# Performance work log

Hardware: AMD Instinct MI355X
Metric: run time of the kernel (lower is better)

Reference implementation:

```python
import jax, jax.numpy as jnp
import numpy as np

N_BUS = 4096
BATCH = 1024


def setup_inputs() -> dict:
    key = jax.random.key(0)
    ks = jax.random.split(key, 10)
    u = jax.random.normal(ks[0], (BATCH, N_BUS), dtype=jnp.float32)
    w = jax.random.normal(ks[1], (BATCH, N_BUS), dtype=jnp.float32)
    # parameters (torch.rand -> uniform[0,1); Linear init ~ U(-1/sqrt(n), 1/sqrt(n)))
    G = jax.random.uniform(ks[2], (N_BUS, N_BUS), dtype=jnp.float32)
    B = jax.random.uniform(ks[3], (N_BUS, N_BUS), dtype=jnp.float32)
    bias_p = jax.random.uniform(ks[4], (1, N_BUS), dtype=jnp.float32)
    bias_q = jax.random.uniform(ks[5], (1, N_BUS), dtype=jnp.float32)
    lim = 1.0 / np.sqrt(N_BUS)
    Wp = jax.random.uniform(ks[6], (N_BUS, N_BUS), dtype=jnp.float32, minval=-lim, maxval=lim)
    bp = jax.random.uniform(ks[7], (N_BUS,), dtype=jnp.float32, minval=-lim, maxval=lim)
    Wq = jax.random.uniform(ks[8], (N_BUS, N_BUS), dtype=jnp.float32, minval=-lim, maxval=lim)
    bq = jax.random.uniform(ks[9], (N_BUS,), dtype=jnp.float32, minval=-lim, maxval=lim)
    return {"u": u, "w": w, "G": G, "B": B, "bias_p": bias_p, "bias_q": bias_q,
            "Wp": Wp, "bp": bp, "Wq": Wq, "bq": bq}


def reference(u, w, G, B, bias_p, bias_q, Wp, bp, Wq, bq):
    # Algebraically identical to the original's outer-product form:
    # p_i = sum_k (u_i u_k + w_i w_k) G_ik + (w_i u_k - u_i w_k) B_ik
    #     = u_i (G u)_i + w_i (G w)_i + w_i (B u)_i - u_i (B w)_i
    # q_i = sum_k (w_i u_k - u_i w_k) G_ik - (u_i u_k + w_i w_k) B_ik
    #     = w_i (G u)_i - u_i (G w)_i - u_i (B u)_i - w_i (B w)_i
    Gu = u @ G.T  # (batch, n_bus): (G u)_i = sum_k G_ik u_k
    Gw = w @ G.T
    Bu = u @ B.T
    Bw = w @ B.T
    p = u * Gu + w * Gw + w * Bu - u * Bw + bias_p
    q = w * Gu - u * Gw - u * Bu - w * Bw + bias_q
    # nn.Linear: y = x @ W^T + b
    p = p @ Wp.T + bp
    q = q @ Wq.T + bq
    return (p, q)
```

## Files before the change

kernel.cpp:

```cpp
#include <hip/hip_runtime.h>
#include <hip/hip_bf16.h>

#define NB 4096
#define MB 1024
#define SZ ((size_t)MB * NB)
#define NN ((size_t)NB * NB)

typedef __bf16 bf16_t;
typedef __attribute__((ext_vector_type(8))) __bf16 bf16x8;
typedef __attribute__((ext_vector_type(4))) float f32x4;
typedef __attribute__((ext_vector_type(4))) unsigned int u32x4;

#define AS1 __attribute__((address_space(1)))
#define AS3 __attribute__((address_space(3)))
#define GLOAD16(gp, lp)                                                        \
  __builtin_amdgcn_global_load_lds((const AS1 unsigned int*)(gp),              \
                                   (AS3 unsigned int*)(lp), 16, 0, 0)
#define SBAR() __builtin_amdgcn_s_barrier()
#define SCHEDB() __builtin_amdgcn_sched_barrier(0)
#define MFMA16(a, b, c) __builtin_amdgcn_mfma_f32_16x16x32_bf16((a), (b), (c), 0, 0, 0)
#define VMCNT4() asm volatile("s_waitcnt vmcnt(4)" ::: "memory")
#define VMCNT0() asm volatile("s_waitcnt vmcnt(0)" ::: "memory")


__device__ __forceinline__ bf16x8 neg8(bf16x8 x) {
  u32x4 t;
  __builtin_memcpy(&t, &x, 16);
  t ^= 0x80008000u;
  bf16x8 y;
  __builtin_memcpy(&y, &t, 16);
  return y;
}

__device__ __forceinline__ bf16x8 cvt8(float4 a, float4 b) {
  bf16x8 v;
  v[0] = (bf16_t)a.x; v[1] = (bf16_t)a.y; v[2] = (bf16_t)a.z; v[3] = (bf16_t)a.w;
  v[4] = (bf16_t)b.x; v[5] = (bf16_t)b.y; v[6] = (bf16_t)b.z; v[7] = (bf16_t)b.w;
  return v;
}

#define ITEM_S (SZ / 8)
#define ITEM_N (NN / 8)

__global__ __launch_bounds__(256) void prep6_kernel(
    const float* __restrict__ u, const float* __restrict__ w,
    const float* __restrict__ G, const float* __restrict__ Bm,
    const float* __restrict__ Wp, const float* __restrict__ Wq,
    bf16_t* __restrict__ ws) {
  size_t stride = (size_t)gridDim.x * blockDim.x;
  const size_t tot = 2 * ITEM_S + 4 * ITEM_N;
  for (size_t i = (size_t)blockIdx.x * blockDim.x + threadIdx.x; i < tot;
       i += stride) {
    const float* src;
    bf16_t* dst;
    size_t off;
    if (i < ITEM_S) { src = u; dst = ws; off = i; }
    else if (i < 2 * ITEM_S) { src = w; dst = ws + SZ; off = i - ITEM_S; }
    else if (i < 2 * ITEM_S + ITEM_N) { src = G; dst = ws + 2 * SZ; off = i - 2 * ITEM_S; }
    else if (i < 2 * ITEM_S + 2 * ITEM_N) { src = Bm; dst = ws + 2 * SZ + NN; off = i - 2 * ITEM_S - ITEM_N; }
    else if (i < 2 * ITEM_S + 3 * ITEM_N) { src = Wp; dst = ws + 2 * SZ + 2 * NN; off = i - 2 * ITEM_S - 2 * ITEM_N; }
    else { src = Wq; dst = ws + 2 * SZ + 3 * NN; off = i - 2 * ITEM_S - 3 * ITEM_N; }
    const float4* s = reinterpret_cast<const float4*>(src) + off * 2;
    reinterpret_cast<bf16x8*>(dst)[off] = cvt8(s[0], s[1]);
  }
}

__global__ __launch_bounds__(256) void prep4_kernel(
    const float* __restrict__ u, const float* __restrict__ w,
    const float* __restrict__ G, const float* __restrict__ Bm,
    bf16_t* __restrict__ ws) {
  size_t stride = (size_t)gridDim.x * blockDim.x;
  const size_t tot = 2 * ITEM_S + 2 * ITEM_N;
  for (size_t i = (size_t)blockIdx.x * blockDim.x + threadIdx.x; i < tot;
       i += stride) {
    const float* src;
    bf16_t* dst;
    size_t off;
    if (i < ITEM_S) { src = u; dst = ws; off = i; }
    else if (i < 2 * ITEM_S) { src = w; dst = ws + SZ; off = i - ITEM_S; }
    else if (i < 2 * ITEM_S + ITEM_N) { src = G; dst = ws + 2 * SZ; off = i - 2 * ITEM_S; }
    else { src = Bm; dst = ws + 2 * SZ + NN; off = i - 2 * ITEM_S - ITEM_N; }
    const float4* s = reinterpret_cast<const float4*>(src) + off * 2;
    reinterpret_cast<bf16x8*>(dst)[off] = cvt8(s[0], s[1]);
  }
}

__global__ __launch_bounds__(256, 2) void fused1_v9(
    const float* __restrict__ u, const float* __restrict__ w,
    const bf16_t* __restrict__ ubf, const bf16_t* __restrict__ wbf,
    const bf16_t* __restrict__ Gbf, const bf16_t* __restrict__ Bbf,
    const float* __restrict__ bias_p, const float* __restrict__ bias_q,
    bf16_t* __restrict__ pq) {
  __shared__ bf16_t lds[2][4][128 * 32];
  const int tid = threadIdx.x, lane = tid & 63, wv = tid >> 6;
  const int bid = blockIdx.x;
  const int t = (bid & 7) * 32 + (bid >> 3);
  const int row0 = (t & 7) * 128, col0 = (t >> 3) * 128;
  const int koff = (bid & 1) << 6;
  const int wm = (wv >> 1) * 64, wn = (wv & 1) * 64;
  const int lr = lane & 15, kq = lane >> 4;
  const int kswz = (kq ^ ((lr >> 1) & 3)) << 3;

  const int srow = tid >> 2;
  const int sc = (tid & 3) ^ ((tid >> 3) & 3);
  const bf16_t* gsA[4];
  const bf16_t* gsB[4];
  {
    const bf16_t* bases[4] = {ubf, wbf, Gbf, Bbf};
    const int r0s[4] = {row0, row0, col0, col0};
#pragma unroll
    for (int o = 0; o < 4; ++o) {
      gsA[o] = bases[o] + (size_t)(r0s[o] + srow) * NB + sc * 8;
      gsB[o] = gsA[o] + (size_t)64 * NB;
    }
  }

#define F1_ISSUE(hh)                                                          \
  do {                                                                        \
    const int _sl = (hh) & 1;                                                 \
    const int _ko = (((hh) + koff) & 127) * 32;                               \
    _Pragma("unroll") for (int _o = 0; _o < 4; ++_o) {                        \
      GLOAD16(gsA[_o] + _ko, &lds[_sl][_o][wv * 512]);                        \
      GLOAD16(gsB[_o] + _ko, &lds[_sl][_o][2048 + wv * 512]);                 \
    }                                                                         \
  } while (0)

  int aoff[4], boff[4];
#pragma unroll
  for (int m = 0; m < 4; ++m) aoff[m] = (wm + m * 16 + lr) * 32 + kswz;
#pragma unroll
  for (int n = 0; n < 4; ++n) boff[n] = (wn + n * 16 + lr) * 32 + kswz;

  f32x4 aS[4][4] = {}, aT[4][4] = {};

  F1_ISSUE(0);
  VMCNT0();
  __syncthreads();

  for (int h = 0; h < 128; ++h) {
    const int slot = h & 1;
    bf16x8 au[4], aw[4], bG[4], bB[4];
#pragma unroll
    for (int m = 0; m < 4; ++m) {
      au[m] = *reinterpret_cast<const bf16x8*>(&lds[slot][0][aoff[m]]);
      aw[m] = *reinterpret_cast<const bf16x8*>(&lds[slot][1][aoff[m]]);
    }
#pragma unroll
    for (int n = 0; n < 4; ++n) {
      bG[n] = *reinterpret_cast<const bf16x8*>(&lds[slot][2][boff[n]]);
      bB[n] = *reinterpret_cast<const bf16x8*>(&lds[slot][3][boff[n]]);
    }
    if (h + 1 < 128) F1_ISSUE(h + 1);
#pragma unroll
    for (int n = 0; n < 4; ++n) {
      bf16x8 bn = neg8(bB[n]);
#pragma unroll
      for (int m = 0; m < 4; ++m) {
        aS[m][n] = MFMA16(au[m], bG[n], aS[m][n]);
        aS[m][n] = MFMA16(aw[m], bn, aS[m][n]);
        aT[m][n] = MFMA16(aw[m], bG[n], aT[m][n]);
        aT[m][n] = MFMA16(au[m], bB[n], aT[m][n]);
      }
    }
    if (h + 1 < 128) {
      VMCNT0();
      SBAR();
      SCHEDB();
    }
  }

  const int fr = lane & 15, fq = kq;
#pragma unroll
  for (int m = 0; m < 4; ++m)
#pragma unroll
    for (int n = 0; n < 4; ++n)
#pragma unroll
      for (int j = 0; j < 4; ++j) {
        int r = row0 + wm + m * 16 + fq * 4 + j;
        int c = col0 + wn + n * 16 + fr;
        size_t idx = (size_t)r * NB + c;
        float U = u[idx], W = w[idx];
        float S = aS[m][n][j], T = aT[m][n][j];
        pq[idx] = (bf16_t)(U * S + W * T + bias_p[c]);
        pq[SZ + idx] = (bf16_t)(W * S - U * T + bias_q[c]);
      }
}

__global__ __launch_bounds__(256, 2) void gemm2_v9(
    const bf16_t* __restrict__ pq, const bf16_t* __restrict__ Wpb,
    const bf16_t* __restrict__ Wqb, const float* __restrict__ bp,
    const float* __restrict__ bq, float* __restrict__ out) {
  __shared__ bf16_t lds[4][2][128 * 32];
  const int tid = threadIdx.x, lane = tid & 63, wv = tid >> 6;
  const int bid = blockIdx.x;
  const int t = (bid & 7) * 64 + (bid >> 3);
  const int z = t >> 8;
  const int s = t & 255;
  const int row0 = (s & 7) * 128, col0 = (s >> 3) * 128;
  const int koff = (bid & 1) << 6;

  const bf16_t* A = pq + (size_t)z * SZ;
  const bf16_t* Wm = z ? Wqb : Wpb;
  const float* bias = z ? bq : bp;
  float* C = out + (size_t)z * SZ;

  const int wm = (wv >> 1) * 64, wn = (wv & 1) * 64;
  const int lr = lane & 15, kq = lane >> 4;
  const int kswz = (kq ^ ((lr >> 1) & 3)) << 3;

  const int srow = tid >> 2;
  const int sc = (tid & 3) ^ ((tid >> 3) & 3);
  const bf16_t* gA0 = A + (size_t)(row0 + srow) * NB + sc * 8;
  const bf16_t* gA1 = gA0 + (size_t)64 * NB;
  const bf16_t* gW0 = Wm + (size_t)(col0 + srow) * NB + sc * 8;
  const bf16_t* gW1 = gW0 + (size_t)64 * NB;

#define G2_ISSUE(hh)                                                           \
  do {                                                                         \
    const int _sl = (hh) & 3;                                                  \
    const int _ko = (((hh) + koff) & 127) * 32;                                \
    GLOAD16(gA0 + _ko, &lds[_sl][0][wv * 512]);                                \
    GLOAD16(gA1 + _ko, &lds[_sl][0][2048 + wv * 512]);                         \
    GLOAD16(gW0 + _ko, &lds[_sl][1][wv * 512]);                                \
    GLOAD16(gW1 + _ko, &lds[_sl][1][2048 + wv * 512]);                         \
  } while (0)

  int aoff[4], woff[4];
#pragma unroll
  for (int m = 0; m < 4; ++m) aoff[m] = (wm + m * 16 + lr) * 32 + kswz;
#pragma unroll
  for (int n = 0; n < 4; ++n) woff[n] = (wn + n * 16 + lr) * 32 + kswz;

  f32x4 acc[4][4] = {};

  G2_ISSUE(0); G2_ISSUE(1); G2_ISSUE(2);
  VMCNT4();
  SBAR();
  SCHEDB();

  const int HTOT = 2 * (NB / 64);
  for (int h = 0; h < HTOT; ++h) {
    const int slot = h & 3;
    const bool pf = (h + 3) < HTOT;

    bf16x8 av[4], bw[4];
#pragma unroll
    for (int m = 0; m < 4; ++m)
      av[m] = *reinterpret_cast<const bf16x8*>(&lds[slot][0][aoff[m]]);
#pragma unroll
    for (int n = 0; n < 4; ++n)
      bw[n] = *reinterpret_cast<const bf16x8*>(&lds[slot][1][woff[n]]);
    if (pf) G2_ISSUE(h + 3);
#pragma unroll
    for (int m = 0; m < 4; ++m)
#pragma unroll
      for (int n = 0; n < 4; ++n)
        acc[m][n] = MFMA16(av[m], bw[n], acc[m][n]);
    if (h < HTOT - 3)
      VMCNT4();
    else if (h == HTOT - 3)
      asm volatile("s_waitcnt vmcnt(2)" ::: "memory");
    else if (h == HTOT - 2)
      VMCNT0();
    SBAR();
    SCHEDB();
  }

  const int fr = lane & 15, fq = kq;
#pragma unroll
  for (int m = 0; m < 4; ++m)
#pragma unroll
    for (int n = 0; n < 4; ++n)
#pragma unroll
      for (int j = 0; j < 4; ++j) {
        int r = row0 + wm + m * 16 + fq * 4 + j;
        int c = col0 + wn + n * 16 + fr;
        C[(size_t)r * NB + c] = acc[m][n][j] + bias[c];
      }
}

__device__ __forceinline__ int swz_off32(int r, int kk) {
  return r * 32 + ((kk ^ ((r >> 1) & 3)) << 3);
}

__device__ __forceinline__ void fb_stage_f32(const float* __restrict__ src,
                                             int row0, int k0, bf16_t* lds, int t) {
  int r = t >> 2, kk = t & 3;
  const float* p = src + (size_t)(row0 + r) * NB + k0 + (kk << 3);
  float4 v0 = *reinterpret_cast<const float4*>(p);
  float4 v1 = *reinterpret_cast<const float4*>(p + 4);
  *reinterpret_cast<bf16x8*>(lds + swz_off32(r, kk)) = cvt8(v0, v1);
}

__global__ __launch_bounds__(256, 2) void fb_gemm2(
    const bf16_t* __restrict__ pq, const float* __restrict__ Wp,
    const float* __restrict__ Wq, const float* __restrict__ bp,
    const float* __restrict__ bq, float* __restrict__ out) {
  __shared__ bf16_t lA[128 * 32], lW[128 * 32];
  const int z = blockIdx.z;
  const bf16_t* A = pq + (size_t)z * SZ;
  const float* Wm = z ? Wq : Wp;
  const float* bias = z ? bq : bp;
  float* C = out + (size_t)z * SZ;
  const int tid = threadIdx.x;
  const int lane = tid & 63, wv = tid >> 6;
  const int wm = (wv >> 1) * 64, wn = (wv & 1) * 64;
  const int row0 = blockIdx.y * 128, col0 = blockIdx.x * 128;
  const int lr = lane & 15, kq = lane >> 4;
  const int fslot = (kq ^ ((lr >> 1) & 3)) << 3;
  f32x4 acc[4][4] = {};
  for (int kt = 0; kt < NB; kt += 32) {
#pragma unroll
    for (int p = 0; p < 2; ++p) {
      int cb = p * 256 + wv * 64;
      int ci = cb + lane;
      int r = ci >> 2, kl = ci & 3;
      int ks = kl ^ ((r >> 1) & 3);
      const bf16_t* g = A + (size_t)(row0 + r) * NB + kt + (ks << 3);
      GLOAD16(g, lA + cb * 8);
    }
#pragma unroll
    for (int p = 0; p < 2; ++p)
      fb_stage_f32(Wm, col0, kt, lW, p * 256 + tid);
    __syncthreads();
    bf16x8 af[4], bg[4];
#pragma unroll
    for (int m = 0; m < 4; ++m)
      af[m] = *reinterpret_cast<const bf16x8*>(lA + (wm + m * 16 + lr) * 32 + fslot);
#pragma unroll
    for (int n = 0; n < 4; ++n)
      bg[n] = *reinterpret_cast<const bf16x8*>(lW + (wn + n * 16 + lr) * 32 + fslot);
#pragma unroll
    for (int m = 0; m < 4; ++m)
#pragma unroll
      for (int n = 0; n < 4; ++n)
        acc[m][n] = MFMA16(af[m], bg[n], acc[m][n]);
    __syncthreads();
  }
  const int fr = lane & 15, fq = lane >> 4;
#pragma unroll
  for (int m = 0; m < 4; ++m)
#pragma unroll
    for (int n = 0; n < 4; ++n)
#pragma unroll
      for (int j = 0; j < 4; ++j) {
        int r = row0 + wm + m * 16 + fq * 4 + j;
        int c = col0 + wn + n * 16 + fr;
        C[(size_t)r * NB + c] = acc[m][n][j] + bias[c];
      }
}

__global__ __launch_bounds__(512, 2) void fb_fused1(
    const float* __restrict__ u, const float* __restrict__ w,
    const float* __restrict__ G, const float* __restrict__ Bm,
    const float* __restrict__ bias_p, const float* __restrict__ bias_q,
    bf16_t* __restrict__ pq) {
  __shared__ bf16_t lU[128 * 32], lW[128 * 32], lG[128 * 32], lB[128 * 32];
  const int tid = threadIdx.x;
  const int lane = tid & 63, wv = tid >> 6;
  const int wm = (wv >> 2) * 64, wn = (wv & 3) * 32;
  const int row0 = blockIdx.y * 128, col0 = blockIdx.x * 128;
  const int lr = lane & 15, kq = lane >> 4;
  const int fslot = (kq ^ ((lr >> 1) & 3)) << 3;
  f32x4 aS[4][2] = {}, aT[4][2] = {};
  for (int kt = 0; kt < NB; kt += 32) {
    fb_stage_f32(u, row0, kt, lU, tid);
    fb_stage_f32(w, row0, kt, lW, tid);
    fb_stage_f32(G, col0, kt, lG, tid);
    fb_stage_f32(Bm, col0, kt, lB, tid);
    __syncthreads();
    bf16x8 au[4], aw[4], bG[2], bB[2], bBn[2];
#pragma unroll
    for (int m = 0; m < 4; ++m) {
      int off = (wm + m * 16 + lr) * 32 + fslot;
      au[m] = *reinterpret_cast<const bf16x8*>(lU + off);
      aw[m] = *reinterpret_cast<const bf16x8*>(lW + off);
    }
#pragma unroll
    for (int n = 0; n < 2; ++n) {
      int off = (wn + n * 16 + lr) * 32 + fslot;
      bG[n] = *reinterpret_cast<const bf16x8*>(lG + off);
      bB[n] = *reinterpret_cast<const bf16x8*>(lB + off);
      bBn[n] = neg8(bB[n]);
    }
#pragma unroll
    for (int m = 0; m < 4; ++m)
#pragma unroll
      for (int n = 0; n < 2; ++n) {
        aS[m][n] = MFMA16(au[m], bG[n], aS[m][n]);
        aS[m][n] = MFMA16(aw[m], bBn[n], aS[m][n]);
        aT[m][n] = MFMA16(aw[m], bG[n], aT[m][n]);
        aT[m][n] = MFMA16(au[m], bB[n], aT[m][n]);
      }
    __syncthreads();
  }
  const int fr = lane & 15, fq = lane >> 4;
#pragma unroll
  for (int m = 0; m < 4; ++m)
#pragma unroll
    for (int n = 0; n < 2; ++n)
#pragma unroll
      for (int j = 0; j < 4; ++j) {
        int r = row0 + wm + m * 16 + fq * 4 + j;
        int c = col0 + wn + n * 16 + fr;
        size_t idx = (size_t)r * NB + c;
        float U = u[idx], W = w[idx];
        float S = aS[m][n][j], T = aT[m][n][j];
        pq[idx] = (bf16_t)(U * S + W * T + bias_p[c]);
        pq[SZ + idx] = (bf16_t)(W * S - U * T + bias_q[c]);
      }
}

extern "C" void kernel_launch(void* const* d_in, const int* in_sizes, int n_in,
                              void* d_out, int out_size, void* d_ws, size_t ws_size,
                              hipStream_t stream) {
  const float* u = (const float*)d_in[0];
  const float* w = (const float*)d_in[1];
  const float* G = (const float*)d_in[2];
  const float* Bm = (const float*)d_in[3];
  const float* bias_p = (const float*)d_in[4];
  const float* bias_q = (const float*)d_in[5];
  const float* Wp = (const float*)d_in[6];
  const float* bp = (const float*)d_in[7];
  const float* Wq = (const float*)d_in[8];
  const float* bq = (const float*)d_in[9];
  (void)in_sizes; (void)n_in; (void)out_size;

  const size_t need_full = (6 * SZ + 4 * NN) * sizeof(bf16_t);
  const size_t need_mid = (6 * SZ + 2 * NN) * sizeof(bf16_t);

  if (ws_size >= need_full) {
    bf16_t* ws = (bf16_t*)d_ws;
    bf16_t* ubf = ws;
    bf16_t* wbf = ws + SZ;
    bf16_t* Gbf = ws + 2 * SZ;
    bf16_t* Bbf = Gbf + NN;
    bf16_t* Wpb = Bbf + NN;
    bf16_t* Wqb = Wpb + NN;
    bf16_t* pqw = Wqb + NN;
    prep6_kernel<<<2048, 256, 0, stream>>>(u, w, G, Bm, Wp, Wq, ws);
    fused1_v9<<<256, 256, 0, stream>>>(u, w, ubf, wbf, Gbf, Bbf,
                                       bias_p, bias_q, pqw);
    gemm2_v9<<<512, 256, 0, stream>>>(pqw, Wpb, Wqb, bp, bq, (float*)d_out);
  } else if (ws_size >= need_mid) {
    bf16_t* ws = (bf16_t*)d_ws;
    bf16_t* ubf = ws;
    bf16_t* wbf = ws + SZ;
    bf16_t* Gbf = ws + 2 * SZ;
    bf16_t* Bbf = Gbf + NN;
    bf16_t* pqw = Bbf + NN;
    prep4_kernel<<<2048, 256, 0, stream>>>(u, w, G, Bm, ws);
    fused1_v9<<<256, 256, 0, stream>>>(u, w, ubf, wbf, Gbf, Bbf,
                                       bias_p, bias_q, pqw);
    fb_gemm2<<<dim3(NB / 128, MB / 128, 2), 256, 0, stream>>>(
        pqw, Wp, Wq, bp, bq, (float*)d_out);
  } else {
    bf16_t* pqw = (bf16_t*)d_ws;
    fb_fused1<<<dim3(NB / 128, MB / 128), 512, 0, stream>>>(
        u, w, G, Bm, bias_p, bias_q, pqw);
    fb_gemm2<<<dim3(NB / 128, MB / 128, 2), 256, 0, stream>>>(
        pqw, Wp, Wq, bp, bq, (float*)d_out);
  }
}
```

Measured before the change: 367.0 us.

## Deepen fused1 LDS pipeline to four stages with prefetch distance three

The first fused GEMM kernel moves from a double-buffered LDS pipeline that waits for all loads every iteration to a four-slot ring buffer. Loads are issued three iterations ahead with partial vmcnt waits. Occupancy drops to one block per CU because the LDS footprint doubles to 128KB. The per-block K-offset rotation (koff) that staggered memory access across blocks is also removed. The aim is to hide global-load latency behind MFMA work, at the cost of fewer resident waves and possibly more contention from aligned accesses.

```diff
diff --git a/kernel.cpp b/kernel.cpp
--- a/kernel.cpp
+++ b/kernel.cpp
@@ -19,8 +19,7 @@
 #define SBAR() __builtin_amdgcn_s_barrier()
 #define SCHEDB() __builtin_amdgcn_sched_barrier(0)
 #define MFMA16(a, b, c) __builtin_amdgcn_mfma_f32_16x16x32_bf16((a), (b), (c), 0, 0, 0)
-#define VMCNT4() asm volatile("s_waitcnt vmcnt(4)" ::: "memory")
-#define VMCNT0() asm volatile("s_waitcnt vmcnt(0)" ::: "memory")
+#define VMCNT(n) asm volatile("s_waitcnt vmcnt(" #n ")" ::: "memory")
 
 
 __device__ __forceinline__ bf16x8 neg8(bf16x8 x) {
@@ -85,18 +84,17 @@
   }
 }
 
-__global__ __launch_bounds__(256, 2) void fused1_v9(
+__global__ __launch_bounds__(256, 1) void fused1_v10(
     const float* __restrict__ u, const float* __restrict__ w,
     const bf16_t* __restrict__ ubf, const bf16_t* __restrict__ wbf,
     const bf16_t* __restrict__ Gbf, const bf16_t* __restrict__ Bbf,
     const float* __restrict__ bias_p, const float* __restrict__ bias_q,
     bf16_t* __restrict__ pq) {
-  __shared__ bf16_t lds[2][4][128 * 32];
+  __shared__ bf16_t lds[4][4][128 * 32];
   const int tid = threadIdx.x, lane = tid & 63, wv = tid >> 6;
   const int bid = blockIdx.x;
   const int t = (bid & 7) * 32 + (bid >> 3);
   const int row0 = (t & 7) * 128, col0 = (t >> 3) * 128;
-  const int koff = (bid & 1) << 6;
   const int wm = (wv >> 1) * 64, wn = (wv & 1) * 64;
   const int lr = lane & 15, kq = lane >> 4;
   const int kswz = (kq ^ ((lr >> 1) & 3)) << 3;
@@ -117,8 +115,8 @@
 
 #define F1_ISSUE(hh)                                                          \
   do {                                                                        \
-    const int _sl = (hh) & 1;                                                 \
-    const int _ko = (((hh) + koff) & 127) * 32;                               \
+    const int _sl = (hh) & 3;                                                 \
+    const int _ko = (hh) * 32;                                                \
     _Pragma("unroll") for (int _o = 0; _o < 4; ++_o) {                        \
       GLOAD16(gsA[_o] + _ko, &lds[_sl][_o][wv * 512]);                        \
       GLOAD16(gsB[_o] + _ko, &lds[_sl][_o][2048 + wv * 512]);                 \
@@ -133,12 +131,13 @@
 
   f32x4 aS[4][4] = {}, aT[4][4] = {};
 
-  F1_ISSUE(0);
-  VMCNT0();
-  __syncthreads();
+  F1_ISSUE(0); F1_ISSUE(1); F1_ISSUE(2);
+  VMCNT(16);
+  SBAR();
+  SCHEDB();
 
   for (int h = 0; h < 128; ++h) {
-    const int slot = h & 1;
+    const int slot = h & 3;
     bf16x8 au[4], aw[4], bG[4], bB[4];
 #pragma unroll
     for (int m = 0; m < 4; ++m) {
@@ -150,7 +149,7 @@
       bG[n] = *reinterpret_cast<const bf16x8*>(&lds[slot][2][boff[n]]);
       bB[n] = *reinterpret_cast<const bf16x8*>(&lds[slot][3][boff[n]]);
     }
-    if (h + 1 < 128) F1_ISSUE(h + 1);
+    if (h + 3 < 128) F1_ISSUE(h + 3);
 #pragma unroll
     for (int n = 0; n < 4; ++n) {
       bf16x8 bn = neg8(bB[n]);
@@ -162,8 +161,16 @@
         aT[m][n] = MFMA16(au[m], bB[n], aT[m][n]);
       }
     }
-    if (h + 1 < 128) {
-      VMCNT0();
+    if (h <= 124) {
+      VMCNT(16);
+      SBAR();
+      SCHEDB();
+    } else if (h == 125) {
+      VMCNT(8);
+      SBAR();
+      SCHEDB();
+    } else if (h == 126) {
+      VMCNT(0);
       SBAR();
       SCHEDB();
     }
@@ -234,7 +241,7 @@
   f32x4 acc[4][4] = {};
 
   G2_ISSUE(0); G2_ISSUE(1); G2_ISSUE(2);
-  VMCNT4();
+  VMCNT(4);
   SBAR();
   SCHEDB();
 
@@ -257,11 +264,11 @@
       for (int n = 0; n < 4; ++n)
         acc[m][n] = MFMA16(av[m], bw[n], acc[m][n]);
     if (h < HTOT - 3)
-      VMCNT4();
+      VMCNT(4);
     else if (h == HTOT - 3)
-      asm volatile("s_waitcnt vmcnt(2)" ::: "memory");
+      VMCNT(2);
     else if (h == HTOT - 2)
-      VMCNT0();
+      VMCNT(0);
     SBAR();
     SCHEDB();
   }
@@ -439,8 +446,8 @@
     bf16_t* Wqb = Wpb + NN;
     bf16_t* pqw = Wqb + NN;
     prep6_kernel<<<2048, 256, 0, stream>>>(u, w, G, Bm, Wp, Wq, ws);
-    fused1_v9<<<256, 256, 0, stream>>>(u, w, ubf, wbf, Gbf, Bbf,
-                                       bias_p, bias_q, pqw);
+    fused1_v10<<<256, 256, 0, stream>>>(u, w, ubf, wbf, Gbf, Bbf,
+                                        bias_p, bias_q, pqw);
     gemm2_v9<<<512, 256, 0, stream>>>(pqw, Wpb, Wqb, bp, bq, (float*)d_out);
   } else if (ws_size >= need_mid) {
     bf16_t* ws = (bf16_t*)d_ws;
@@ -450,8 +457,8 @@
     bf16_t* Bbf = Gbf + NN;
     bf16_t* pqw = Bbf + NN;
     prep4_kernel<<<2048, 256, 0, stream>>>(u, w, G, Bm, ws);
-    fused1_v9<<<256, 256, 0, stream>>>(u, w, ubf, wbf, Gbf, Bbf,
-                                       bias_p, bias_q, pqw);
+    fused1_v10<<<256, 256, 0, stream>>>(u, w, ubf, wbf, Gbf, Bbf,
+                                        bias_p, bias_q, pqw);
     fb_gemm2<<<dim3(NB / 128, MB / 128, 2), 256, 0, stream>>>(
         pqw, Wp, Wq, bp, bq, (float*)d_out);
   } else {
```

Result: faster. 308.3 us (-16.0%).
